# Optimization experiments

Measured on AMD Instinct MI355X. Metric: run time of the kernel, lower is better.

## Reference

```python
import jax, jax.numpy as jnp
import numpy as np


def _get_rel_pos(q_size, k_size, rel_pos):
    # table length is assumed == 2*max(q,k)-1 (no interpolation path)
    q_coords = jnp.arange(q_size)[:, None] * max(k_size / q_size, 1.0)
    k_coords = jnp.arange(k_size)[None, :] * max(q_size / k_size, 1.0)
    rel = (q_coords - k_coords + (k_size - 1) * max(q_size / k_size, 1.0)).astype(jnp.int32)
    return rel_pos[rel]  # (q_size, k_size, head_dim)


def setup_inputs() -> dict:
    key = jax.random.key(0)
    ks = jax.random.split(key, 7)
    B, N, C = 8, 1024, 768
    s = 0.02
    return {
        "x": jax.random.normal(ks[0], (B, N, C), jnp.float32),
        "qkv_w": jax.random.normal(ks[1], (3 * C, C), jnp.float32) * s,
        "qkv_b": jax.random.normal(ks[2], (3 * C,), jnp.float32) * s,
        "proj_w": jax.random.normal(ks[3], (C, C), jnp.float32) * s,
        "proj_b": jax.random.normal(ks[4], (C,), jnp.float32) * s,
        "rel_pos_h": jax.random.normal(ks[5], (63, 64), jnp.float32) * s,
        "rel_pos_w": jax.random.normal(ks[6], (63, 64), jnp.float32) * s,
        "H": 32,
        "W": 32,
    }


def reference(x, qkv_w, qkv_b, proj_w, proj_b, rel_pos_h, rel_pos_w, H, W):
    B, N, C = x.shape
    hd = rel_pos_h.shape[-1]
    nh = C // hd
    scale = hd ** -0.5

    qkv = (x @ qkv_w.T + qkv_b).reshape(B, N, 3, nh, hd)
    q, k, v = [qkv[:, :, i].transpose(0, 2, 1, 3) for i in range(3)]  # (B, nh, N, hd)

    # decomposed relative position bias on the last H*W query/key tokens (here all of them)
    Rh = _get_rel_pos(H, H, rel_pos_h)  # (H, H, hd)
    Rw = _get_rel_pos(W, W, rel_pos_w)  # (W, W, hd)
    r_q = q.reshape(B * nh, H, W, hd)
    rel_h = jnp.einsum("bhwc,hkc->bhwk", r_q, Rh)  # (B*nh, H, W, H)
    rel_w = jnp.einsum("bhwc,wkc->bhwk", r_q, Rw)  # (B*nh, H, W, W)
    bias = (rel_h[..., :, None] + rel_w[..., None, :]).reshape(B, nh, N, N)

    scores = jnp.einsum("bhqd,bhkd->bhqk", q * scale, k) + bias
    attn = jax.nn.softmax(scores, axis=-1)
    out = jnp.einsum("bhqk,bhkd->bhqd", attn, v)  # (B, nh, N, hd)
    out = out.transpose(0, 2, 1, 3).reshape(B, N, C)
    out = out @ proj_w.T + proj_b

    pre_kv = jnp.stack([k.reshape(B * nh, N, hd), v.reshape(B * nh, N, hd)])
    return out, pre_kv
```

## Files before the change

kernel.cpp:

```cpp
#include <hip/hip_runtime.h>
#include <hip/hip_bf16.h>
#include <stdint.h>

typedef __attribute__((ext_vector_type(8))) short bf16x8;
typedef __attribute__((ext_vector_type(4))) float f32x4;

__device__ __forceinline__ void gload_lds16(const void* g, void* l) {
  typedef __attribute__((address_space(1))) void gv_t;
  typedef __attribute__((address_space(3))) void lv_t;
  __builtin_amdgcn_global_load_lds((gv_t*)(uintptr_t)g,
                                   (lv_t*)(uint32_t)(uintptr_t)l, 16, 0, 0);
}

__global__ __launch_bounds__(256) void cvt_bf16(const float* __restrict__ src,
                                                __hip_bfloat16* __restrict__ dst, int n4) {
  int i = blockIdx.x * 256 + threadIdx.x;
  if (i < n4) {
    float4 f = ((const float4*)src)[i];
    union { ushort4 u; __hip_bfloat16 h[4]; } pk;
    pk.h[0] = __float2bfloat16(f.x);
    pk.h[1] = __float2bfloat16(f.y);
    pk.h[2] = __float2bfloat16(f.z);
    pk.h[3] = __float2bfloat16(f.w);
    ((ushort4*)dst)[i] = pk.u;
  }
}

__global__ __launch_bounds__(256) void cvt_bf16_pad(const float* __restrict__ src,
                                                    __hip_bfloat16* __restrict__ dst,
                                                    int n4src, int n4tot) {
  int i = blockIdx.x * 256 + threadIdx.x;
  if (i < n4tot) {
    float4 f = (i < n4src) ? ((const float4*)src)[i] : make_float4(0.f, 0.f, 0.f, 0.f);
    union { ushort4 u; __hip_bfloat16 h[4]; } pk;
    pk.h[0] = __float2bfloat16(f.x);
    pk.h[1] = __float2bfloat16(f.y);
    pk.h[2] = __float2bfloat16(f.z);
    pk.h[3] = __float2bfloat16(f.w);
    ((ushort4*)dst)[i] = pk.u;
  }
}

__device__ __forceinline__ void gemm_tile_compute(const __hip_bfloat16* __restrict__ A,
                                                  const __hip_bfloat16* __restrict__ Bm,
                                                  int K, int bm, int bn,
                                                  f32x4 acc[4][4], char* lbase) {
  const int tid = threadIdx.x;
  const int lane = tid & 63, w = tid >> 6;
  const int wr = w >> 1, wc = w & 1;
  const int rrow = lane & 15, g16 = lane >> 4;

  for (int k0 = 0; k0 < K; k0 += 32) {
    #pragma unroll
    for (int i = 0; i < 2; ++i) {
      int c = i * 4 + w;
      int b = c * 1024 + (lane << 4);
      int row = b >> 6;
      int cbs = ((b >> 4) & 3) ^ (row & 3);
      const char* ga = (const char*)(A + (size_t)(bm * 128 + row) * K + k0) + cbs * 16;
      gload_lds16(ga, lbase + c * 1024);
      const char* gb = (const char*)(Bm + (size_t)(bn * 128 + row) * K + k0) + cbs * 16;
      gload_lds16(gb, lbase + 8192 + c * 1024);
    }
    asm volatile("s_waitcnt vmcnt(0)" ::: "memory");
    __syncthreads();

    bf16x8 af[4], bfr[4];
    #pragma unroll
    for (int i = 0; i < 4; ++i) {
      int row = wr * 64 + i * 16 + rrow;
      af[i] = *(const bf16x8*)(lbase + row * 64 + ((g16 * 16) ^ ((row & 3) << 4)));
      int col = wc * 64 + i * 16 + rrow;
      bfr[i] = *(const bf16x8*)(lbase + 8192 + col * 64 + ((g16 * 16) ^ ((col & 3) << 4)));
    }
    #pragma unroll
    for (int i = 0; i < 4; ++i)
      #pragma unroll
      for (int j = 0; j < 4; ++j)
        acc[i][j] = __builtin_amdgcn_mfma_f32_16x16x32_bf16(af[i], bfr[j], acc[i][j], 0, 0, 0);
    __syncthreads();
  }
}

__global__ __launch_bounds__(256) void gemm_qkv_kernel(
    const __hip_bfloat16* __restrict__ xb, const __hip_bfloat16* __restrict__ wqkv,
    const float* __restrict__ qkv_b,
    __hip_bfloat16* __restrict__ Qws, __hip_bfloat16* __restrict__ Kws,
    __hip_bfloat16* __restrict__ Vws, float* __restrict__ prekv) {
  __shared__ char smem[16384];
  f32x4 acc[4][4];
  const f32x4 z4 = {0.f, 0.f, 0.f, 0.f};
  #pragma unroll
  for (int i = 0; i < 4; ++i)
    #pragma unroll
    for (int j = 0; j < 4; ++j) acc[i][j] = z4;

  const int bn = blockIdx.x, bm = blockIdx.y;
  gemm_tile_compute(xb, wqkv, 768, bm, bn, acc, smem);

  const int lane = threadIdx.x & 63, w = threadIdx.x >> 6;
  const int wr = w >> 1, wc = w & 1;
  const int col0 = lane & 15, g = lane >> 4;
  #pragma unroll
  for (int j = 0; j < 4; ++j) {
    int n = bn * 128 + wc * 64 + j * 16 + col0;
    float bias = qkv_b[n];
    int which = n / 768;
    int head = (n >> 6) % 12;
    int d = n & 63;
    #pragma unroll
    for (int i = 0; i < 4; ++i) {
      #pragma unroll
      for (int r = 0; r < 4; ++r) {
        int m = bm * 128 + wr * 64 + i * 16 + g * 4 + r;
        float v = acc[i][j][r] + bias;
        int b = m >> 10, t = m & 1023;
        size_t idx = ((size_t)(b * 12 + head) << 16) + (t << 6) + d;
        __hip_bfloat16 hv = __float2bfloat16(v);
        if (which == 0) {
          Qws[idx] = hv;
        } else if (which == 1) {
          Kws[idx] = hv; prekv[idx] = v;
        } else {
          Vws[idx] = hv; prekv[6291456 + idx] = v;
        }
      }
    }
  }
}

__global__ __launch_bounds__(256) void gemm_proj_kernel(
    const __hip_bfloat16* __restrict__ Ows, const __hip_bfloat16* __restrict__ wproj,
    const float* __restrict__ proj_b, float* __restrict__ out) {
  __shared__ char smem[16384];
  f32x4 acc[4][4];
  const f32x4 z4 = {0.f, 0.f, 0.f, 0.f};
  #pragma unroll
  for (int i = 0; i < 4; ++i)
    #pragma unroll
    for (int j = 0; j < 4; ++j) acc[i][j] = z4;

  const int bn = blockIdx.x, bm = blockIdx.y;
  gemm_tile_compute(Ows, wproj, 768, bm, bn, acc, smem);

  const int lane = threadIdx.x & 63, w = threadIdx.x >> 6;
  const int wr = w >> 1, wc = w & 1;
  const int col0 = lane & 15, g = lane >> 4;
  #pragma unroll
  for (int j = 0; j < 4; ++j) {
    int n = bn * 128 + wc * 64 + j * 16 + col0;
    float bias = proj_b[n];
    #pragma unroll
    for (int i = 0; i < 4; ++i) {
      #pragma unroll
      for (int r = 0; r < 4; ++r) {
        int m = bm * 128 + wr * 64 + i * 16 + g * 4 + r;
        out[(size_t)m * 768 + n] = acc[i][j][r] + bias;
      }
    }
  }
}

__global__ __launch_bounds__(256) void flash_attn(
    const __hip_bfloat16* __restrict__ Qws, const __hip_bfloat16* __restrict__ Kws,
    const __hip_bfloat16* __restrict__ Vws, const __hip_bfloat16* __restrict__ rphb,
    const __hip_bfloat16* __restrict__ rpwb, __hip_bfloat16* __restrict__ Ows) {
  __shared__ alignas(16) float s_relh[128 * 32];
  __shared__ alignas(16) float s_relw[128 * 32];
  __shared__ alignas(16) char s_kt[8192];
  __shared__ alignas(16) char s_vt[8192];
  __shared__ alignas(16) char s_pt[16384];

  const int tid = threadIdx.x, lane = tid & 63, w = tid >> 6;
  const int g16 = lane >> 4, c16 = lane & 15;
  const int bid = blockIdx.x;
  const int bh = bid >> 3, qt = bid & 7;
  const int q0 = qt * 128;
  const size_t bhbase = (size_t)bh << 16;

  bf16x8 qf[2][2];
  {
    const __hip_bfloat16* qp = Qws + bhbase + (size_t)(q0 + w * 32 + c16) * 64 + g16 * 8;
    qf[0][0] = *(const bf16x8*)qp;
    qf[0][1] = *(const bf16x8*)(qp + 32);
    qf[1][0] = *(const bf16x8*)(qp + 16 * 64);
    qf[1][1] = *(const bf16x8*)(qp + 16 * 64 + 32);
  }

  const f32x4 z4 = {0.f, 0.f, 0.f, 0.f};

  {
    f32x4 gh[2][4], gw[2][4];
    #pragma unroll
    for (int mb = 0; mb < 2; ++mb)
      #pragma unroll
      for (int nf = 0; nf < 4; ++nf) { gh[mb][nf] = z4; gw[mb][nf] = z4; }
    #pragma unroll
    for (int kc = 0; kc < 2; ++kc) {
      #pragma unroll
      for (int nf = 0; nf < 4; ++nf) {
        int j = nf * 16 + c16;
        const __hip_bfloat16* tp = rphb + j * 64 + kc * 32 + g16 * 8;
        bf16x8 th = *(const bf16x8*)tp;
        bf16x8 tw = *(const bf16x8*)(rpwb + j * 64 + kc * 32 + g16 * 8);
        gh[0][nf] = __builtin_amdgcn_mfma_f32_16x16x32_bf16(qf[0][kc], th, gh[0][nf], 0, 0, 0);
        gh[1][nf] = __builtin_amdgcn_mfma_f32_16x16x32_bf16(qf[1][kc], th, gh[1][nf], 0, 0, 0);
        gw[0][nf] = __builtin_amdgcn_mfma_f32_16x16x32_bf16(qf[0][kc], tw, gw[0][nf], 0, 0, 0);
        gw[1][nf] = __builtin_amdgcn_mfma_f32_16x16x32_bf16(qf[1][kc], tw, gw[1][nf], 0, 0, 0);
      }
    }
    const int hq = (q0 >> 5) + w;
    #pragma unroll
    for (int mb = 0; mb < 2; ++mb) {
      #pragma unroll
      for (int nf = 0; nf < 4; ++nf) {
        int j = nf * 16 + c16;
        int khh = hq - j + 31;
        #pragma unroll
        for (int r = 0; r < 4; ++r) {
          int rowin = mb * 16 + g16 * 4 + r;
          int lrow = w * 32 + rowin;
          if (khh >= 0 && khh < 32) s_relh[lrow * 32 + khh] = gh[mb][nf][r];
          int kww = rowin - j + 31;
          if (kww >= 0 && kww < 32) s_relw[lrow * 32 + kww] = gw[mb][nf][r];
        }
      }
    }
  }

  f32x4 o[2][4];
  float m_r[2][4], l_r[2][4];
  #pragma unroll
  for (int rb = 0; rb < 2; ++rb) {
    #pragma unroll
    for (int hf = 0; hf < 4; ++hf) o[rb][hf] = z4;
    #pragma unroll
    for (int r = 0; r < 4; ++r) { m_r[rb][r] = -1e30f; l_r[rb][r] = 0.f; }
  }

  __syncthreads();

  const float scale = 0.125f;
  for (int kt0 = 0; kt0 < 1024; kt0 += 64) {
    #pragma unroll
    for (int i = 0; i < 2; ++i) {
      int c = w * 2 + i;
      int b = c * 1024 + (lane << 4);
      int row = b >> 7;
      int cbs = ((b >> 4) & 7) ^ (row & 7);
      const char* g = (const char*)(Kws + bhbase + (size_t)(kt0 + row) * 64) + cbs * 16;
      gload_lds16(g, s_kt + c * 1024);
    }
    #pragma unroll
    for (int i = 0; i < 2; ++i) {
      int e = (i * 256 + tid) * 8;
      int key = e >> 6, hd0 = e & 63;
      bf16x8 vv = *(const bf16x8*)(Vws + bhbase + (size_t)(kt0 + key) * 64 + hd0);
      #pragma unroll
      for (int j = 0; j < 8; ++j) {
        int hd = hd0 + j;
        int byte = hd * 128 + ((key * 2) ^ ((hd & 7) << 4));
        *(short*)(s_vt + byte) = vv[j];
      }
    }
    asm volatile("s_waitcnt vmcnt(0)" ::: "memory");
    __syncthreads();

    f32x4 s[2][4];
    #pragma unroll
    for (int rb = 0; rb < 2; ++rb)
      #pragma unroll
      for (int kf = 0; kf < 4; ++kf) s[rb][kf] = z4;
    #pragma unroll
    for (int kc = 0; kc < 2; ++kc) {
      #pragma unroll
      for (int kf = 0; kf < 4; ++kf) {
        int key = kf * 16 + c16;
        int byte = key * 128 + (((kc * 32 + g16 * 8) * 2) ^ ((key & 7) << 4));
        bf16x8 kfr = *(const bf16x8*)(s_kt + byte);
        s[0][kf] = __builtin_amdgcn_mfma_f32_16x16x32_bf16(qf[0][kc], kfr, s[0][kf], 0, 0, 0);
        s[1][kf] = __builtin_amdgcn_mfma_f32_16x16x32_bf16(qf[1][kc], kfr, s[1][kf], 0, 0, 0);
      }
    }

    #pragma unroll
    for (int rb = 0; rb < 2; ++rb) {
      #pragma unroll
      for (int kf = 0; kf < 4; ++kf) {
        int kh = (kt0 >> 5) + (kf >> 1);
        int kw = ((kf & 1) << 4) + c16;
        #pragma unroll
        for (int r = 0; r < 4; ++r) {
          int lrow = w * 32 + rb * 16 + g16 * 4 + r;
          s[rb][kf][r] = s[rb][kf][r] * scale + s_relh[lrow * 32 + kh] + s_relw[lrow * 32 + kw];
        }
      }
      #pragma unroll
      for (int r = 0; r < 4; ++r) {
        float tm = fmaxf(fmaxf(s[rb][0][r], s[rb][1][r]), fmaxf(s[rb][2][r], s[rb][3][r]));
        tm = fmaxf(tm, __shfl_xor(tm, 1));
        tm = fmaxf(tm, __shfl_xor(tm, 2));
        tm = fmaxf(tm, __shfl_xor(tm, 4));
        tm = fmaxf(tm, __shfl_xor(tm, 8));
        float mnew = fmaxf(m_r[rb][r], tm);
        float fac = __expf(m_r[rb][r] - mnew);
        m_r[rb][r] = mnew;
        float psum = 0.f;
        #pragma unroll
        for (int kf = 0; kf < 4; ++kf) {
          float p = __expf(s[rb][kf][r] - mnew);
          s[rb][kf][r] = p;
          psum += p;
        }
        psum += __shfl_xor(psum, 1);
        psum += __shfl_xor(psum, 2);
        psum += __shfl_xor(psum, 4);
        psum += __shfl_xor(psum, 8);
        l_r[rb][r] = l_r[rb][r] * fac + psum;
        #pragma unroll
        for (int hf = 0; hf < 4; ++hf) o[rb][hf] *= fac;
      }
      #pragma unroll
      for (int kf = 0; kf < 4; ++kf) {
        int key = kf * 16 + c16;
        #pragma unroll
        for (int r = 0; r < 4; ++r) {
          int prow = rb * 16 + g16 * 4 + r;
          int byte = w * 4096 + prow * 128 + ((key * 2) ^ ((prow & 7) << 4));
          *(__hip_bfloat16*)(s_pt + byte) = __float2bfloat16(s[rb][kf][r]);
        }
      }
    }
    __syncthreads();

    #pragma unroll
    for (int kc = 0; kc < 2; ++kc) {
      bf16x8 pf[2];
      #pragma unroll
      for (int rb = 0; rb < 2; ++rb) {
        int prow = rb * 16 + c16;
        int byte = w * 4096 + prow * 128 + (((kc * 32 + g16 * 8) * 2) ^ ((prow & 7) << 4));
        pf[rb] = *(const bf16x8*)(s_pt + byte);
      }
      #pragma unroll
      for (int hf = 0; hf < 4; ++hf) {
        int hd = hf * 16 + c16;
        int byte = hd * 128 + (((kc * 32 + g16 * 8) * 2) ^ ((hd & 7) << 4));
        bf16x8 vf = *(const bf16x8*)(s_vt + byte);
        o[0][hf] = __builtin_amdgcn_mfma_f32_16x16x32_bf16(pf[0], vf, o[0][hf], 0, 0, 0);
        o[1][hf] = __builtin_amdgcn_mfma_f32_16x16x32_bf16(pf[1], vf, o[1][hf], 0, 0, 0);
      }
    }
    __syncthreads();
  }

  const int b = bh / 12, head = bh % 12;
  #pragma unroll
  for (int rb = 0; rb < 2; ++rb) {
    #pragma unroll
    for (int r = 0; r < 4; ++r) {
      int row = q0 + w * 32 + rb * 16 + g16 * 4 + r;
      float inv = 1.0f / l_r[rb][r];
      size_t base = ((size_t)b * 1024 + row) * 768 + head * 64;
      #pragma unroll
      for (int hf = 0; hf < 4; ++hf)
        Ows[base + hf * 16 + c16] = __float2bfloat16(o[rb][hf][r] * inv);
    }
  }
}

extern "C" void kernel_launch(void* const* d_in, const int* in_sizes, int n_in,
                              void* d_out, int out_size, void* d_ws, size_t ws_size,
                              hipStream_t stream) {
  const float* x      = (const float*)d_in[0];
  const float* qkv_w  = (const float*)d_in[1];
  const float* qkv_b  = (const float*)d_in[2];
  const float* proj_w = (const float*)d_in[3];
  const float* proj_b = (const float*)d_in[4];
  const float* rph    = (const float*)d_in[5];
  const float* rpw    = (const float*)d_in[6];

  char* ws = (char*)d_ws;
  __hip_bfloat16* xb    = (__hip_bfloat16*)(ws);
  __hip_bfloat16* wqkv  = (__hip_bfloat16*)(ws + 12582912);
  __hip_bfloat16* wproj = (__hip_bfloat16*)(ws + 16121856);
  __hip_bfloat16* Qws   = (__hip_bfloat16*)(ws + 17301504);
  __hip_bfloat16* Kws   = (__hip_bfloat16*)(ws + 29884416);
  __hip_bfloat16* Vws   = (__hip_bfloat16*)(ws + 42467328);
  __hip_bfloat16* rphb  = (__hip_bfloat16*)(ws + 55050240);
  __hip_bfloat16* rpwb  = (__hip_bfloat16*)(ws + 55058432);
  __hip_bfloat16* Ows   = xb;

  float* out   = (float*)d_out;
  float* prekv = out + 6291456;

  cvt_bf16<<<6144, 256, 0, stream>>>(x, xb, 1572864);
  cvt_bf16<<<1728, 256, 0, stream>>>(qkv_w, wqkv, 442368);
  cvt_bf16<<<576, 256, 0, stream>>>(proj_w, wproj, 147456);
  cvt_bf16_pad<<<4, 256, 0, stream>>>(rph, rphb, 1008, 1024);
  cvt_bf16_pad<<<4, 256, 0, stream>>>(rpw, rpwb, 1008, 1024);
  gemm_qkv_kernel<<<dim3(18, 64), 256, 0, stream>>>(xb, wqkv, qkv_b, Qws, Kws, Vws, prekv);
  flash_attn<<<768, 256, 0, stream>>>(Qws, Kws, Vws, rphb, rpwb, Ows);
  gemm_proj_kernel<<<dim3(6, 64), 256, 0, stream>>>(Ows, wproj, proj_b, out);
}
```

Baseline: 333.2 us.

## Store QKV row-major, split prekv conversion, and streamline flash attention loop

The QKV GEMM now writes one row-major bf16 buffer with coalesced stores instead of scattered per-head Q/K/V and fp32 prekv stores. A separate kernel rebuilds prekv from the bf16 values, so pre_kv loses precision because it previously held the fp32 GEMM output. Flash attention reads from the strided buffer and folds log2e into the scale and rel-pos tables so it can use raw v_exp_f32. It also stages V through registers with packed LDS writes, caches the rel_w bias in registers, skips the O rescale when the max is unchanged, merges LDS into one buffer with a launch-bounds occupancy hint, and adds setprio around MFMA blocks.

```diff
diff --git a/kernel.cpp b/kernel.cpp
--- a/kernel.cpp
+++ b/kernel.cpp
@@ -4,6 +4,18 @@
 
 typedef __attribute__((ext_vector_type(8))) short bf16x8;
 typedef __attribute__((ext_vector_type(4))) float f32x4;
+
+#define LOG2E 1.4426950408889634f
+
+__device__ __forceinline__ float exp2_fast(float x) {
+  float r; asm("v_exp_f32 %0, %1" : "=v"(r) : "v"(x)); return r;
+}
+
+__device__ __forceinline__ float bf16bits_to_f32(short h) {
+  union { uint32_t u; float f; } c;
+  c.u = ((uint32_t)(unsigned short)h) << 16;
+  return c.f;
+}
 
 __device__ __forceinline__ void gload_lds16(const void* g, void* l) {
   typedef __attribute__((address_space(1))) void gv_t;
@@ -28,17 +40,44 @@
 
 __global__ __launch_bounds__(256) void cvt_bf16_pad(const float* __restrict__ src,
                                                     __hip_bfloat16* __restrict__ dst,
-                                                    int n4src, int n4tot) {
+                                                    int n4src, int n4tot, float scale) {
   int i = blockIdx.x * 256 + threadIdx.x;
   if (i < n4tot) {
     float4 f = (i < n4src) ? ((const float4*)src)[i] : make_float4(0.f, 0.f, 0.f, 0.f);
     union { ushort4 u; __hip_bfloat16 h[4]; } pk;
-    pk.h[0] = __float2bfloat16(f.x);
-    pk.h[1] = __float2bfloat16(f.y);
-    pk.h[2] = __float2bfloat16(f.z);
-    pk.h[3] = __float2bfloat16(f.w);
+    pk.h[0] = __float2bfloat16(f.x * scale);
+    pk.h[1] = __float2bfloat16(f.y * scale);
+    pk.h[2] = __float2bfloat16(f.z * scale);
+    pk.h[3] = __float2bfloat16(f.w * scale);
     ((ushort4*)dst)[i] = pk.u;
   }
+}
+
+__global__ __launch_bounds__(256) void cvt_prekv(const __hip_bfloat16* __restrict__ xqkv,
+                                                 float* __restrict__ prekv) {
+  int gid = blockIdx.x * 256 + threadIdx.x;
+  int o8 = gid * 8;
+  int which = (o8 >= 6291456) ? 1 : 0;
+  int r = o8 - which * 6291456;
+  int bh = r >> 16;
+  int t  = (r >> 6) & 1023;
+  int d0 = r & 63;
+  int b = bh / 12, h = bh - b * 12;
+  const __hip_bfloat16* src = xqkv + (size_t)(b * 1024 + t) * 2304 +
+                              (which ? 1536 : 768) + h * 64 + d0;
+  bf16x8 v = *(const bf16x8*)src;
+  float* dst = prekv + o8;
+  float4 lo, hi;
+  lo.x = bf16bits_to_f32(v[0]);
+  lo.y = bf16bits_to_f32(v[1]);
+  lo.z = bf16bits_to_f32(v[2]);
+  lo.w = bf16bits_to_f32(v[3]);
+  hi.x = bf16bits_to_f32(v[4]);
+  hi.y = bf16bits_to_f32(v[5]);
+  hi.z = bf16bits_to_f32(v[6]);
+  hi.w = bf16bits_to_f32(v[7]);
+  *(float4*)dst = lo;
+  *(float4*)(dst + 4) = hi;
 }
 
 __device__ __forceinline__ void gemm_tile_compute(const __hip_bfloat16* __restrict__ A,
@@ -73,20 +112,20 @@
       int col = wc * 64 + i * 16 + rrow;
       bfr[i] = *(const bf16x8*)(lbase + 8192 + col * 64 + ((g16 * 16) ^ ((col & 3) << 4)));
     }
+    __builtin_amdgcn_s_setprio(1);
     #pragma unroll
     for (int i = 0; i < 4; ++i)
       #pragma unroll
       for (int j = 0; j < 4; ++j)
         acc[i][j] = __builtin_amdgcn_mfma_f32_16x16x32_bf16(af[i], bfr[j], acc[i][j], 0, 0, 0);
+    __builtin_amdgcn_s_setprio(0);
     __syncthreads();
   }
 }
 
 __global__ __launch_bounds__(256) void gemm_qkv_kernel(
     const __hip_bfloat16* __restrict__ xb, const __hip_bfloat16* __restrict__ wqkv,
-    const float* __restrict__ qkv_b,
-    __hip_bfloat16* __restrict__ Qws, __hip_bfloat16* __restrict__ Kws,
-    __hip_bfloat16* __restrict__ Vws, float* __restrict__ prekv) {
+    const float* __restrict__ qkv_b, __hip_bfloat16* __restrict__ xqkv) {
   __shared__ char smem[16384];
   f32x4 acc[4][4];
   const f32x4 z4 = {0.f, 0.f, 0.f, 0.f};
@@ -105,25 +144,12 @@
   for (int j = 0; j < 4; ++j) {
     int n = bn * 128 + wc * 64 + j * 16 + col0;
     float bias = qkv_b[n];
-    int which = n / 768;
-    int head = (n >> 6) % 12;
-    int d = n & 63;
     #pragma unroll
     for (int i = 0; i < 4; ++i) {
       #pragma unroll
       for (int r = 0; r < 4; ++r) {
         int m = bm * 128 + wr * 64 + i * 16 + g * 4 + r;
-        float v = acc[i][j][r] + bias;
-        int b = m >> 10, t = m & 1023;
-        size_t idx = ((size_t)(b * 12 + head) << 16) + (t << 6) + d;
-        __hip_bfloat16 hv = __float2bfloat16(v);
-        if (which == 0) {
-          Qws[idx] = hv;
-        } else if (which == 1) {
-          Kws[idx] = hv; prekv[idx] = v;
-        } else {
-          Vws[idx] = hv; prekv[6291456 + idx] = v;
-        }
+        xqkv[(size_t)m * 2304 + n] = __float2bfloat16(acc[i][j][r] + bias);
       }
     }
   }
@@ -161,30 +187,34 @@
   }
 }
 
-__global__ __launch_bounds__(256) void flash_attn(
-    const __hip_bfloat16* __restrict__ Qws, const __hip_bfloat16* __restrict__ Kws,
-    const __hip_bfloat16* __restrict__ Vws, const __hip_bfloat16* __restrict__ rphb,
+#define VSWZ(hd) ((((hd) ^ ((hd) >> 3)) & 7) << 4)
+__global__ __launch_bounds__(256, 3) void flash_attn(
+    const __hip_bfloat16* __restrict__ xqkv, const __hip_bfloat16* __restrict__ rphb,
     const __hip_bfloat16* __restrict__ rpwb, __hip_bfloat16* __restrict__ Ows) {
-  __shared__ alignas(16) float s_relh[128 * 32];
-  __shared__ alignas(16) float s_relw[128 * 32];
-  __shared__ alignas(16) char s_kt[8192];
-  __shared__ alignas(16) char s_vt[8192];
-  __shared__ alignas(16) char s_pt[16384];
+  __shared__ alignas(16) char smem[49152];
+  float* s_relh = (float*)smem;
+  char*  s_kt   = smem + 16384;
+  char*  s_vt   = smem + 24576;
+  char*  s_pt   = smem + 32768;
+  float* s_rw   = (float*)(smem + 32768);
 
   const int tid = threadIdx.x, lane = tid & 63, w = tid >> 6;
   const int g16 = lane >> 4, c16 = lane & 15;
   const int bid = blockIdx.x;
-  const int bh = bid >> 3, qt = bid & 7;
+  const int qt = bid / 96, bh = bid - qt * 96;
   const int q0 = qt * 128;
-  const size_t bhbase = (size_t)bh << 16;
+  const int b = bh / 12, head = bh - b * 12;
+  const __hip_bfloat16* Qb = xqkv + (size_t)b * 1024 * 2304 + head * 64;
+  const __hip_bfloat16* Kb = Qb + 768;
+  const __hip_bfloat16* Vb = Qb + 1536;
 
   bf16x8 qf[2][2];
   {
-    const __hip_bfloat16* qp = Qws + bhbase + (size_t)(q0 + w * 32 + c16) * 64 + g16 * 8;
+    const __hip_bfloat16* qp = Qb + (size_t)(q0 + w * 32 + c16) * 2304 + g16 * 8;
     qf[0][0] = *(const bf16x8*)qp;
     qf[0][1] = *(const bf16x8*)(qp + 32);
-    qf[1][0] = *(const bf16x8*)(qp + 16 * 64);
-    qf[1][1] = *(const bf16x8*)(qp + 16 * 64 + 32);
+    qf[1][0] = *(const bf16x8*)(qp + 16 * 2304);
+    qf[1][1] = *(const bf16x8*)(qp + 16 * 2304 + 32);
   }
 
   const f32x4 z4 = {0.f, 0.f, 0.f, 0.f};
@@ -200,8 +230,7 @@
       #pragma unroll
       for (int nf = 0; nf < 4; ++nf) {
         int j = nf * 16 + c16;
-        const __hip_bfloat16* tp = rphb + j * 64 + kc * 32 + g16 * 8;
-        bf16x8 th = *(const bf16x8*)tp;
+        bf16x8 th = *(const bf16x8*)(rphb + j * 64 + kc * 32 + g16 * 8);
         bf16x8 tw = *(const bf16x8*)(rpwb + j * 64 + kc * 32 + g16 * 8);
         gh[0][nf] = __builtin_amdgcn_mfma_f32_16x16x32_bf16(qf[0][kc], th, gh[0][nf], 0, 0, 0);
         gh[1][nf] = __builtin_amdgcn_mfma_f32_16x16x32_bf16(qf[1][kc], th, gh[1][nf], 0, 0, 0);
@@ -222,11 +251,21 @@
           int lrow = w * 32 + rowin;
           if (khh >= 0 && khh < 32) s_relh[lrow * 32 + khh] = gh[mb][nf][r];
           int kww = rowin - j + 31;
-          if (kww >= 0 && kww < 32) s_relw[lrow * 32 + kww] = gw[mb][nf][r];
+          if (kww >= 0 && kww < 32) s_rw[lrow * 32 + kww] = gw[mb][nf][r];
         }
       }
     }
   }
+  asm volatile("s_waitcnt lgkmcnt(0)" ::: "memory");
+  float rw0[2][4], rw1[2][4];
+  #pragma unroll
+  for (int rb = 0; rb < 2; ++rb)
+    #pragma unroll
+    for (int r = 0; r < 4; ++r) {
+      int lrow = w * 32 + rb * 16 + g16 * 4 + r;
+      rw0[rb][r] = s_rw[lrow * 32 + c16];
+      rw1[rb][r] = s_rw[lrow * 32 + 16 + c16];
+    }
 
   f32x4 o[2][4];
   float m_r[2][4], l_r[2][4];
@@ -238,39 +277,32 @@
     for (int r = 0; r < 4; ++r) { m_r[rb][r] = -1e30f; l_r[rb][r] = 0.f; }
   }
 
-  __syncthreads();
-
-  const float scale = 0.125f;
+  const float SCALE2 = 0.125f * LOG2E;
+  const int kp = tid >> 3;
+  const int hd0 = (tid & 7) * 8;
+
   for (int kt0 = 0; kt0 < 1024; kt0 += 64) {
     #pragma unroll
     for (int i = 0; i < 2; ++i) {
       int c = w * 2 + i;
-      int b = c * 1024 + (lane << 4);
-      int row = b >> 7;
-      int cbs = ((b >> 4) & 7) ^ (row & 7);
-      const char* g = (const char*)(Kws + bhbase + (size_t)(kt0 + row) * 64) + cbs * 16;
+      int row = c * 8 + (lane >> 3);
+      int cbs = (lane & 7) ^ (row & 7);
+      const char* g = (const char*)(Kb + (size_t)(kt0 + row) * 2304) + cbs * 16;
       gload_lds16(g, s_kt + c * 1024);
     }
-    #pragma unroll
-    for (int i = 0; i < 2; ++i) {
-      int e = (i * 256 + tid) * 8;
-      int key = e >> 6, hd0 = e & 63;
-      bf16x8 vv = *(const bf16x8*)(Vws + bhbase + (size_t)(kt0 + key) * 64 + hd0);
-      #pragma unroll
-      for (int j = 0; j < 8; ++j) {
-        int hd = hd0 + j;
-        int byte = hd * 128 + ((key * 2) ^ ((hd & 7) << 4));
-        *(short*)(s_vt + byte) = vv[j];
-      }
-    }
-    asm volatile("s_waitcnt vmcnt(0)" ::: "memory");
-    __syncthreads();
+    asm volatile("" ::: "memory");
+    const __hip_bfloat16* vr = Vb + (size_t)(kt0 + 2 * kp) * 2304 + hd0;
+    bf16x8 va = *(const bf16x8*)vr;
+    bf16x8 vb = *(const bf16x8*)(vr + 2304);
+    asm volatile("s_waitcnt vmcnt(2)" ::: "memory");
+    __builtin_amdgcn_s_barrier();
 
     f32x4 s[2][4];
     #pragma unroll
     for (int rb = 0; rb < 2; ++rb)
       #pragma unroll
       for (int kf = 0; kf < 4; ++kf) s[rb][kf] = z4;
+    __builtin_amdgcn_s_setprio(1);
     #pragma unroll
     for (int kc = 0; kc < 2; ++kc) {
       #pragma unroll
@@ -282,19 +314,36 @@
         s[1][kf] = __builtin_amdgcn_mfma_f32_16x16x32_bf16(qf[1][kc], kfr, s[1][kf], 0, 0, 0);
       }
     }
-
+    __builtin_amdgcn_s_setprio(0);
+
+    asm volatile("s_waitcnt vmcnt(0)" ::: "memory");
+    #pragma unroll
+    for (int j = 0; j < 8; ++j) {
+      int hd = hd0 + j;
+      union { ushort2 u2; uint32_t u; } pk;
+      pk.u2.x = (unsigned short)va[j];
+      pk.u2.y = (unsigned short)vb[j];
+      *(uint32_t*)(s_vt + hd * 128 + ((4 * kp) ^ VSWZ(hd))) = pk.u;
+    }
+
+    int kh0 = kt0 >> 5;
+    f32x4 facv[2];
     #pragma unroll
     for (int rb = 0; rb < 2; ++rb) {
-      #pragma unroll
-      for (int kf = 0; kf < 4; ++kf) {
-        int kh = (kt0 >> 5) + (kf >> 1);
-        int kw = ((kf & 1) << 4) + c16;
+      float rh0[4], rh1[4];
+      #pragma unroll
+      for (int r = 0; r < 4; ++r) {
+        int lrow = w * 32 + rb * 16 + g16 * 4 + r;
+        float2 rh = *(const float2*)&s_relh[lrow * 32 + kh0];
+        rh0[r] = rh.x; rh1[r] = rh.y;
+      }
+      #pragma unroll
+      for (int kf = 0; kf < 4; ++kf)
         #pragma unroll
-        for (int r = 0; r < 4; ++r) {
-          int lrow = w * 32 + rb * 16 + g16 * 4 + r;
-          s[rb][kf][r] = s[rb][kf][r] * scale + s_relh[lrow * 32 + kh] + s_relw[lrow * 32 + kw];
-        }
-      }
+        for (int r = 0; r < 4; ++r)
+          s[rb][kf][r] = fmaf(s[rb][kf][r], SCALE2,
+                              ((kf >> 1) ? rh1[r] : rh0[r]) +
+                              ((kf & 1) ? rw1[rb][r] : rw0[rb][r]));
       #pragma unroll
       for (int r = 0; r < 4; ++r) {
         float tm = fmaxf(fmaxf(s[rb][0][r], s[rb][1][r]), fmaxf(s[rb][2][r], s[rb][3][r]));
@@ -302,13 +351,15 @@
         tm = fmaxf(tm, __shfl_xor(tm, 2));
         tm = fmaxf(tm, __shfl_xor(tm, 4));
         tm = fmaxf(tm, __shfl_xor(tm, 8));
-        float mnew = fmaxf(m_r[rb][r], tm);
-        float fac = __expf(m_r[rb][r] - mnew);
+        float mold = m_r[rb][r];
+        float mnew = fmaxf(mold, tm);
+        float fac = exp2_fast(mold - mnew);
         m_r[rb][r] = mnew;
+        facv[rb][r] = fac;
         float psum = 0.f;
         #pragma unroll
         for (int kf = 0; kf < 4; ++kf) {
-          float p = __expf(s[rb][kf][r] - mnew);
+          float p = exp2_fast(s[rb][kf][r] - mnew);
           s[rb][kf][r] = p;
           psum += p;
         }
@@ -316,10 +367,21 @@
         psum += __shfl_xor(psum, 2);
         psum += __shfl_xor(psum, 4);
         psum += __shfl_xor(psum, 8);
-        l_r[rb][r] = l_r[rb][r] * fac + psum;
+        l_r[rb][r] = fmaf(l_r[rb][r], fac, psum);
+      }
+    }
+    bool nr = (facv[0][0] == 1.f) & (facv[0][1] == 1.f) & (facv[0][2] == 1.f) &
+              (facv[0][3] == 1.f) & (facv[1][0] == 1.f) & (facv[1][1] == 1.f) &
+              (facv[1][2] == 1.f) & (facv[1][3] == 1.f);
+    if (!__all(nr)) {
+      #pragma unroll
+      for (int rb = 0; rb < 2; ++rb)
         #pragma unroll
-        for (int hf = 0; hf < 4; ++hf) o[rb][hf] *= fac;
-      }
+        for (int hf = 0; hf < 4; ++hf) o[rb][hf] *= facv[rb];
+    }
+
+    #pragma unroll
+    for (int rb = 0; rb < 2; ++rb)
       #pragma unroll
       for (int kf = 0; kf < 4; ++kf) {
         int key = kf * 16 + c16;
@@ -330,9 +392,11 @@
           *(__hip_bfloat16*)(s_pt + byte) = __float2bfloat16(s[rb][kf][r]);
         }
       }
-    }
-    __syncthreads();
-
+
+    asm volatile("s_waitcnt lgkmcnt(0)" ::: "memory");
+    __builtin_amdgcn_s_barrier();
+
+    __builtin_amdgcn_s_setprio(1);
     #pragma unroll
     for (int kc = 0; kc < 2; ++kc) {
       bf16x8 pf[2];
@@ -345,16 +409,15 @@
       #pragma unroll
       for (int hf = 0; hf < 4; ++hf) {
         int hd = hf * 16 + c16;
-        int byte = hd * 128 + (((kc * 32 + g16 * 8) * 2) ^ ((hd & 7) << 4));
+        int byte = hd * 128 + (((kc * 32 + g16 * 8) * 2) ^ VSWZ(hd));
         bf16x8 vf = *(const bf16x8*)(s_vt + byte);
         o[0][hf] = __builtin_amdgcn_mfma_f32_16x16x32_bf16(pf[0], vf, o[0][hf], 0, 0, 0);
         o[1][hf] = __builtin_amdgcn_mfma_f32_16x16x32_bf16(pf[1], vf, o[1][hf], 0, 0, 0);
       }
     }
-    __syncthreads();
-  }
-
-  const int b = bh / 12, head = bh % 12;
+    __builtin_amdgcn_s_setprio(0);
+  }
+
   #pragma unroll
   for (int rb = 0; rb < 2; ++rb) {
     #pragma unroll
@@ -384,9 +447,7 @@
   __hip_bfloat16* xb    = (__hip_bfloat16*)(ws);
   __hip_bfloat16* wqkv  = (__hip_bfloat16*)(ws + 12582912);
   __hip_bfloat16* wproj = (__hip_bfloat16*)(ws + 16121856);
-  __hip_bfloat16* Qws   = (__hip_bfloat16*)(ws + 17301504);
-  __hip_bfloat16* Kws   = (__hip_bfloat16*)(ws + 29884416);
-  __hip_bfloat16* Vws   = (__hip_bfloat16*)(ws + 42467328);
+  __hip_bfloat16* xqkv  = (__hip_bfloat16*)(ws + 17301504);
   __hip_bfloat16* rphb  = (__hip_bfloat16*)(ws + 55050240);
   __hip_bfloat16* rpwb  = (__hip_bfloat16*)(ws + 55058432);
   __hip_bfloat16* Ows   = xb;
@@ -397,9 +458,10 @@
   cvt_bf16<<<6144, 256, 0, stream>>>(x, xb, 1572864);
   cvt_bf16<<<1728, 256, 0, stream>>>(qkv_w, wqkv, 442368);
   cvt_bf16<<<576, 256, 0, stream>>>(proj_w, wproj, 147456);
-  cvt_bf16_pad<<<4, 256, 0, stream>>>(rph, rphb, 1008, 1024);
-  cvt_bf16_pad<<<4, 256, 0, stream>>>(rpw, rpwb, 1008, 1024);
-  gemm_qkv_kernel<<<dim3(18, 64), 256, 0, stream>>>(xb, wqkv, qkv_b, Qws, Kws, Vws, prekv);
-  flash_attn<<<768, 256, 0, stream>>>(Qws, Kws, Vws, rphb, rpwb, Ows);
+  cvt_bf16_pad<<<4, 256, 0, stream>>>(rph, rphb, 1008, 1024, LOG2E);
+  cvt_bf16_pad<<<4, 256, 0, stream>>>(rpw, rpwb, 1008, 1024, LOG2E);
+  gemm_qkv_kernel<<<dim3(18, 64), 256, 0, stream>>>(xb, wqkv, qkv_b, xqkv);
+  cvt_prekv<<<6144, 256, 0, stream>>>(xqkv, prekv);
+  flash_attn<<<768, 256, 0, stream>>>(xqkv, rphb, rpwb, Ows);
   gemm_proj_kernel<<<dim3(6, 64), 256, 0, stream>>>(Ows, wproj, proj_b, out);
 }
```

Result: slower. 370.8 us (+11.3%).
